# Optimization experiments

Measured on AMD Instinct MI355X. Metric: run time of the kernel, lower is better.

## Reference

```python
import jax, jax.numpy as jnp
import numpy as np

NQ = 12  # qubits == features of M
# (op, theta_offset_or_control, wire_or_target) mirroring TTN_node_forward
CIRCUIT = [
    ("u3", 0, 0), ("u3", 3, 1), ("cx", 0, 1),
    ("u3", 6, 2), ("u3", 9, 3), ("cx", 3, 2),
    ("u3", 12, 4), ("u3", 15, 5), ("cx", 4, 5),
    ("u3", 18, 6), ("u3", 21, 7), ("cx", 7, 6),
    ("u3", 24, 8), ("u3", 27, 9), ("cx", 8, 9),
    ("u3", 30, 10), ("u3", 33, 11), ("cx", 11, 10),
    ("u3", 36, 1), ("u3", 39, 2), ("cx", 1, 2),
    ("u3", 42, 5), ("u3", 45, 6), ("cx", 6, 5),
    ("u3", 48, 9), ("u3", 51, 10), ("cx", 10, 9),
    ("u3", 54, 2), ("u3", 57, 5), ("cx", 2, 5),
    ("u3", 60, 5), ("u3", 63, 9), ("cx", 5, 9),
    ("u3", 66, 4),
]

def _u3(theta, phi, lam):
    ct, st = jnp.cos(theta / 2), jnp.sin(theta / 2)
    r0 = jnp.stack([ct + 0j, -jnp.exp(1j * lam) * st])
    r1 = jnp.stack([jnp.exp(1j * phi) * st, jnp.exp(1j * (phi + lam)) * ct])
    return jnp.stack([r0, r1])  # [2,2] complex64

def _apply_1q(state, U, w):
    # state: (N, 2, ..., 2) with 12 qubit axes; contract U into axis w+1
    out = jnp.tensordot(U, state, axes=((1,), (w + 1,)))
    return jnp.moveaxis(out, 0, w + 1)

def _apply_cnot(state, c, t):
    c_ax, t_ax = c + 1, t + 1
    s0 = jnp.take(state, 0, axis=c_ax)
    s1 = jnp.take(state, 1, axis=c_ax)
    t_adj = t_ax - 1 if t_ax > c_ax else t_ax
    s1 = jnp.flip(s1, axis=t_adj)  # X on target (size-2 axis flip)
    return jnp.stack([s0, s1], axis=c_ax)

def _simulate(M, theta):
    # M: (N, 12) angles; product state from RY(M[:, q]) |0>
    N = M.shape[0]
    state = jnp.ones((N,), dtype=jnp.complex64)
    for q in range(NQ):
        qv = jnp.stack([jnp.cos(M[:, q] / 2), jnp.sin(M[:, q] / 2)], axis=-1)
        qv = qv.astype(jnp.complex64).reshape((N,) + (1,) * q + (2,))
        state = state[..., None] * qv  # (N, 2^(q+1) as axes)
    for op, a, b in CIRCUIT:
        if op == "u3":
            state = _apply_1q(state, _u3(theta[a], theta[a + 1], theta[a + 2]), b)
        else:
            state = _apply_cnot(state, a, b)
    p = jnp.real(state) ** 2 + jnp.imag(state) ** 2  # probabilities
    sum_axes = tuple(ax for ax in range(1, NQ + 1) if ax != 10)  # keep wire 9
    pz = p.sum(axis=sum_axes)  # (N, 2)
    return pz[:, 0] - pz[:, 1]  # <Z_9>

def setup_inputs() -> dict:
    key = jax.random.key(0)
    k1, k2, k3, k4, k5 = jax.random.split(key, 5)
    N, E = 2048, 4096
    X = jax.random.normal(k1, (N, 4), dtype=jnp.float32)
    e = jax.random.uniform(k2, (E,), dtype=jnp.float32)
    Ri = jax.random.uniform(k3, (N, E), dtype=jnp.float32)
    Ro = jax.random.uniform(k4, (N, E), dtype=jnp.float32)
    theta_learn = jax.random.uniform(k5, (69,), dtype=jnp.float32,
                                     minval=0.0, maxval=2.0 * np.pi)
    return {"X": X, "e": e, "Ri": Ri, "Ro": Ro, "theta_learn": theta_learn}

def reference(X, e, Ri, Ro, theta_learn):
    bo = jnp.einsum('ne,nd->ed', Ro, X)          # Ro^T X
    bi = jnp.einsum('ne,nd->ed', Ri, X)          # Ri^T X
    mi = jnp.einsum('ne,ed->nd', Ri * e[None, :], bo)
    mo = jnp.einsum('ne,ed->nd', Ro * e[None, :], bi)
    M = jnp.concatenate([mi, mo, X], axis=1)     # (N, 12)
    z = _simulate(M, theta_learn)
    return jnp.pi * (1.0 - z)                    # 2*pi*(1 - <Z>)/2
```

## Files before the change

kernel.cpp:

```cpp
#include <hip/hip_runtime.h>
#include <math.h>

#define N_SAMPLES 2048
#define E_EDGES   4096
#define NSPLIT    32

__global__ __launch_bounds__(256) void k_partial(const float* __restrict__ Ri,
                                                 const float* __restrict__ Ro,
                                                 const float* __restrict__ X,
                                                 float* __restrict__ pbo,
                                                 float* __restrict__ pbi) {
    __shared__ float comb[128][33];

    const int ec   = blockIdx.x;
    const int ns   = blockIdx.y;
    const int t    = threadIdx.x;
    const int col  = t & 127;
    const int half = t >> 7;
    const int v    = ec * 128 + col;

    const float4* Ri4 = reinterpret_cast<const float4*>(Ri);
    const float4* Ro4 = reinterpret_cast<const float4*>(Ro);
    const float4* X4  = reinterpret_cast<const float4*>(X);

    float abo[4][4], abi[4][4];
#pragma unroll
    for (int c = 0; c < 4; ++c)
#pragma unroll
        for (int d = 0; d < 4; ++d) { abo[c][d] = 0.f; abi[c][d] = 0.f; }

    const int n0 = ns * 64 + half * 32;
    for (int n = n0; n < n0 + 32; ++n) {
        float4 xv = X4[n];
        float4 ro = Ro4[(size_t)n * 1024 + v];
        float4 ri = Ri4[(size_t)n * 1024 + v];
        float xs[4]  = {xv.x, xv.y, xv.z, xv.w};
        float ros[4] = {ro.x, ro.y, ro.z, ro.w};
        float ris[4] = {ri.x, ri.y, ri.z, ri.w};
#pragma unroll
        for (int c = 0; c < 4; ++c)
#pragma unroll
            for (int d = 0; d < 4; ++d) {
                abo[c][d] += ros[c] * xs[d];
                abi[c][d] += ris[c] * xs[d];
            }
    }

    if (half) {
#pragma unroll
        for (int c = 0; c < 4; ++c)
#pragma unroll
            for (int d = 0; d < 4; ++d) {
                comb[col][c * 4 + d]      = abo[c][d];
                comb[col][16 + c * 4 + d] = abi[c][d];
            }
    }
    __syncthreads();
    if (!half) {
        float4* pbo4 = reinterpret_cast<float4*>(pbo);
        float4* pbi4 = reinterpret_cast<float4*>(pbi);
#pragma unroll
        for (int c = 0; c < 4; ++c) {
#pragma unroll
            for (int d = 0; d < 4; ++d) {
                abo[c][d] += comb[col][c * 4 + d];
                abi[c][d] += comb[col][16 + c * 4 + d];
            }
            size_t idx = (size_t)ns * E_EDGES + 4 * (size_t)v + c;
            pbo4[idx] = make_float4(abo[c][0], abo[c][1], abo[c][2], abo[c][3]);
            pbi4[idx] = make_float4(abi[c][0], abi[c][1], abi[c][2], abi[c][3]);
        }
    }
}

__global__ __launch_bounds__(256) void k_reduce(const float* __restrict__ pbo,
                                                const float* __restrict__ pbi,
                                                const float* __restrict__ ev,
                                                float* __restrict__ boT,
                                                float* __restrict__ biT) {
    const int gid = blockIdx.x * 256 + threadIdx.x;
    const int mat = gid >> 12;
    const int e   = gid & 4095;
    const float4* src = reinterpret_cast<const float4*>(mat ? pbi : pbo);
    float*        dst = mat ? biT : boT;
    double s0 = 0, s1 = 0, s2 = 0, s3 = 0;
    for (int ns = 0; ns < NSPLIT; ++ns) {
        float4 a = src[(size_t)ns * E_EDGES + e];
        s0 += a.x; s1 += a.y; s2 += a.z; s3 += a.w;
    }
    const float w = ev[e];
    dst[0 * E_EDGES + e] = w * (float)s0;
    dst[1 * E_EDGES + e] = w * (float)s1;
    dst[2 * E_EDGES + e] = w * (float)s2;
    dst[3 * E_EDGES + e] = w * (float)s3;
}

__global__ __launch_bounds__(256) void k_sim(const float* __restrict__ Ri,
                                             const float* __restrict__ Ro,
                                             const float* __restrict__ X,
                                             const float* __restrict__ th,
                                             const float* __restrict__ boT,
                                             const float* __restrict__ biT,
                                             float* __restrict__ out) {
    __shared__ double redM[4][8];
    __shared__ float  R[22][9];
    __shared__ float  sM[12], cM[12];

    const int n    = blockIdx.x;
    const int t    = threadIdx.x;
    const int lane = t & 63;
    const int wv   = t >> 6;

    if (t < 22) {
        float T = th[3 * t], P = th[3 * t + 1], L = th[3 * t + 2];
        float st, ct, sp, cp, sl, cl;
        sincosf(T, &st, &ct);
        sincosf(P, &sp, &cp);
        sincosf(L, &sl, &cl);
        R[t][0] =  cp * ct * cl - sp * sl;
        R[t][1] = -cp * ct * sl - sp * cl;
        R[t][2] =  cp * st;
        R[t][3] =  sp * ct * cl + cp * sl;
        R[t][4] = -sp * ct * sl + cp * cl;
        R[t][5] =  sp * st;
        R[t][6] = -st * cl;
        R[t][7] =  st * sl;
        R[t][8] =  ct;
    }

    float accf[8];
#pragma unroll
    for (int j = 0; j < 8; ++j) accf[j] = 0.f;

    const float4* Ri4 = reinterpret_cast<const float4*>(Ri + (size_t)n * E_EDGES);
    const float4* Ro4 = reinterpret_cast<const float4*>(Ro + (size_t)n * E_EDGES);
    const float4* BO0 = reinterpret_cast<const float4*>(boT);
    const float4* BO1 = reinterpret_cast<const float4*>(boT + E_EDGES);
    const float4* BO2 = reinterpret_cast<const float4*>(boT + 2 * E_EDGES);
    const float4* BO3 = reinterpret_cast<const float4*>(boT + 3 * E_EDGES);
    const float4* BI0 = reinterpret_cast<const float4*>(biT);
    const float4* BI1 = reinterpret_cast<const float4*>(biT + E_EDGES);
    const float4* BI2 = reinterpret_cast<const float4*>(biT + 2 * E_EDGES);
    const float4* BI3 = reinterpret_cast<const float4*>(biT + 3 * E_EDGES);
#pragma unroll
    for (int k = 0; k < 4; ++k) {
        const int v = t + 256 * k;
        const float4 ri = Ri4[v], ro = Ro4[v];
        const float4 o0 = BO0[v], o1 = BO1[v], o2 = BO2[v], o3 = BO3[v];
        const float4 i0 = BI0[v], i1 = BI1[v], i2 = BI2[v], i3 = BI3[v];
        accf[0] += ri.x * o0.x + ri.y * o0.y + ri.z * o0.z + ri.w * o0.w;
        accf[1] += ri.x * o1.x + ri.y * o1.y + ri.z * o1.z + ri.w * o1.w;
        accf[2] += ri.x * o2.x + ri.y * o2.y + ri.z * o2.z + ri.w * o2.w;
        accf[3] += ri.x * o3.x + ri.y * o3.y + ri.z * o3.z + ri.w * o3.w;
        accf[4] += ro.x * i0.x + ro.y * i0.y + ro.z * i0.z + ro.w * i0.w;
        accf[5] += ro.x * i1.x + ro.y * i1.y + ro.z * i1.z + ro.w * i1.w;
        accf[6] += ro.x * i2.x + ro.y * i2.y + ro.z * i2.z + ro.w * i2.w;
        accf[7] += ro.x * i3.x + ro.y * i3.y + ro.z * i3.z + ro.w * i3.w;
    }
    double accd[8];
#pragma unroll
    for (int j = 0; j < 8; ++j) accd[j] = (double)accf[j];
#pragma unroll
    for (int off = 32; off >= 1; off >>= 1)
#pragma unroll
        for (int j = 0; j < 8; ++j) accd[j] += __shfl_xor(accd[j], off);
    if (lane == 0)
#pragma unroll
        for (int j = 0; j < 8; ++j) redM[wv][j] = accd[j];
    __syncthreads();

    if (t < 12) {
        double Mw = (t < 8)
            ? (redM[0][t] + redM[1][t] + redM[2][t] + redM[3][t])
            : (double)X[n * 4 + (t - 8)];
        double sv, cv;
        sincos(Mw, &sv, &cv);
        sM[t] = (float)sv; cM[t] = (float)cv;
    }
    __syncthreads();

    if (t == 0) {
        auto iz = [&](int g) -> float {
            return R[g][6] * sM[g] + R[g][8] * cM[g];
        };
        auto ivec = [&](int g, float& x, float& y, float& z) {
            x = R[g][0] * sM[g] + R[g][2] * cM[g];
            y = R[g][3] * sM[g] + R[g][5] * cM[g];
            z = R[g][6] * sM[g] + R[g][8] * cM[g];
        };
        auto rot = [&](int g, float& x, float& y, float& z) {
            float nx = R[g][0] * x + R[g][1] * y + R[g][2] * z;
            float ny = R[g][3] * x + R[g][4] * y + R[g][5] * z;
            float nz = R[g][6] * x + R[g][7] * y + R[g][8] * z;
            x = nx; y = ny; z = nz;
        };

        const float z0  = iz(0),  z3  = iz(3), z4 = iz(4);
        const float z7  = iz(7),  z8  = iz(8), z11 = iz(11);

        float x1, y1, z1;  ivec(1, x1, y1, z1);
        y1 *= z0;  z1 *= z0;          rot(12, x1, y1, z1);

        float x2, y2, z2;  ivec(2, x2, y2, z2);
        y2 *= z3;  z2 *= z3;          rot(13, x2, y2, z2);
        y2 *= z1;  z2 *= z1;          rot(18, x2, y2, z2);

        float x6, y6, z6;  ivec(6, x6, y6, z6);
        y6 *= z7;  z6 *= z7;          rot(15, x6, y6, z6);

        float x5, y5, z5;  ivec(5, x5, y5, z5);
        y5 *= z4;  z5 *= z4;          rot(14, x5, y5, z5);
        y5 *= z6;  z5 *= z6;          rot(19, x5, y5, z5);
        y5 *= z2;  z5 *= z2;          rot(20, x5, y5, z5);

        float xA, yA, zA;  ivec(10, xA, yA, zA);
        yA *= z11; zA *= z11;         rot(17, xA, yA, zA);

        float x9, y9, z9;  ivec(9, x9, y9, z9);
        y9 *= z8;  z9 *= z8;          rot(16, x9, y9, z9);
        y9 *= zA;  z9 *= zA;          rot(21, x9, y9, z9);
        z9 *= z5;

        out[n] = (float)(3.14159265358979323846 * (1.0 - (double)z9));
    }
}

extern "C" void kernel_launch(void* const* d_in, const int* in_sizes, int n_in,
                              void* d_out, int out_size, void* d_ws, size_t ws_size,
                              hipStream_t stream) {
    (void)in_sizes; (void)n_in; (void)out_size; (void)ws_size;
    const float* X  = (const float*)d_in[0];
    const float* ev = (const float*)d_in[1];
    const float* Ri = (const float*)d_in[2];
    const float* Ro = (const float*)d_in[3];
    const float* th = (const float*)d_in[4];
    float* out = (float*)d_out;

    float* pbo = (float*)d_ws;
    float* pbi = pbo + (size_t)NSPLIT * E_EDGES * 4;
    float* boT = pbi + (size_t)NSPLIT * E_EDGES * 4;
    float* biT = boT + (size_t)4 * E_EDGES;

    hipLaunchKernelGGL(k_partial, dim3(8, NSPLIT), dim3(256), 0, stream,
                       Ri, Ro, X, pbo, pbi);
    hipLaunchKernelGGL(k_reduce, dim3(32), dim3(256), 0, stream,
                       pbo, pbi, ev, boT, biT);
    hipLaunchKernelGGL(k_sim, dim3(N_SAMPLES), dim3(256), 0, stream,
                       Ri, Ro, X, th, boT, biT, out);
}
```

Before: 41.13 us.

## Split partial sums finer, parallelize reduce across lanes, batch samples per sim block

Doubles the N-split of the partial Ro^T X / Ri^T X kernel to 64 chunks so more blocks run in parallel. The reduce kernel gets four lanes per edge, each summing 16 partials in float, combined with shuffles; the float accumulation replaces double. The sim kernel now handles four samples per block, loading boT/biT once and reusing them across samples, which cuts redundant reads of the shared vectors. The workspace for partials grows, and the lower-precision reduction may slightly change numerics.

New measurement: 43.13 us. 4.9% more time.

```diff
diff --git a/kernel.cpp b/kernel.cpp
--- a/kernel.cpp
+++ b/kernel.cpp
@@ -3,7 +3,8 @@
 
 #define N_SAMPLES 2048
 #define E_EDGES   4096
-#define NSPLIT    32
+#define NSPLIT    64
+#define SPB       4
 
 __global__ __launch_bounds__(256) void k_partial(const float* __restrict__ Ri,
                                                  const float* __restrict__ Ro,
@@ -29,8 +30,9 @@
 #pragma unroll
         for (int d = 0; d < 4; ++d) { abo[c][d] = 0.f; abi[c][d] = 0.f; }
 
-    const int n0 = ns * 64 + half * 32;
-    for (int n = n0; n < n0 + 32; ++n) {
+    const int n0 = ns * 32 + half * 16;
+#pragma unroll 4
+    for (int n = n0; n < n0 + 16; ++n) {
         float4 xv = X4[n];
         float4 ro = Ro4[(size_t)n * 1024 + v];
         float4 ri = Ri4[(size_t)n * 1024 + v];
@@ -79,20 +81,29 @@
                                                 float* __restrict__ boT,
                                                 float* __restrict__ biT) {
     const int gid = blockIdx.x * 256 + threadIdx.x;
-    const int mat = gid >> 12;
-    const int e   = gid & 4095;
+    const int q   = gid & 3;
+    const int e   = (gid >> 2) & 4095;
+    const int mat = gid >> 14;
     const float4* src = reinterpret_cast<const float4*>(mat ? pbi : pbo);
     float*        dst = mat ? biT : boT;
-    double s0 = 0, s1 = 0, s2 = 0, s3 = 0;
-    for (int ns = 0; ns < NSPLIT; ++ns) {
+
+    float s0 = 0.f, s1 = 0.f, s2 = 0.f, s3 = 0.f;
+#pragma unroll 4
+    for (int ns = q * 16; ns < q * 16 + 16; ++ns) {
         float4 a = src[(size_t)ns * E_EDGES + e];
         s0 += a.x; s1 += a.y; s2 += a.z; s3 += a.w;
     }
-    const float w = ev[e];
-    dst[0 * E_EDGES + e] = w * (float)s0;
-    dst[1 * E_EDGES + e] = w * (float)s1;
-    dst[2 * E_EDGES + e] = w * (float)s2;
-    dst[3 * E_EDGES + e] = w * (float)s3;
+    s0 += __shfl_xor(s0, 1); s0 += __shfl_xor(s0, 2);
+    s1 += __shfl_xor(s1, 1); s1 += __shfl_xor(s1, 2);
+    s2 += __shfl_xor(s2, 1); s2 += __shfl_xor(s2, 2);
+    s3 += __shfl_xor(s3, 1); s3 += __shfl_xor(s3, 2);
+    if (q == 0) {
+        const float w = ev[e];
+        dst[0 * E_EDGES + e] = w * s0;
+        dst[1 * E_EDGES + e] = w * s1;
+        dst[2 * E_EDGES + e] = w * s2;
+        dst[3 * E_EDGES + e] = w * s3;
+    }
 }
 
 __global__ __launch_bounds__(256) void k_sim(const float* __restrict__ Ri,
@@ -102,11 +113,11 @@
                                              const float* __restrict__ boT,
                                              const float* __restrict__ biT,
                                              float* __restrict__ out) {
-    __shared__ double redM[4][8];
+    __shared__ double redM[4][SPB][8];
     __shared__ float  R[22][9];
-    __shared__ float  sM[12], cM[12];
-
-    const int n    = blockIdx.x;
+    __shared__ float  sM[SPB][12], cM[SPB][12];
+
+    const int n0   = blockIdx.x * SPB;
     const int t    = threadIdx.x;
     const int lane = t & 63;
     const int wv   = t >> 6;
@@ -128,12 +139,19 @@
         R[t][8] =  ct;
     }
 
-    float accf[8];
-#pragma unroll
-    for (int j = 0; j < 8; ++j) accf[j] = 0.f;
-
-    const float4* Ri4 = reinterpret_cast<const float4*>(Ri + (size_t)n * E_EDGES);
-    const float4* Ro4 = reinterpret_cast<const float4*>(Ro + (size_t)n * E_EDGES);
+    float accf[SPB][8];
+#pragma unroll
+    for (int s = 0; s < SPB; ++s)
+#pragma unroll
+        for (int j = 0; j < 8; ++j) accf[s][j] = 0.f;
+
+    const float4* Ri4s[SPB];
+    const float4* Ro4s[SPB];
+#pragma unroll
+    for (int s = 0; s < SPB; ++s) {
+        Ri4s[s] = reinterpret_cast<const float4*>(Ri + (size_t)(n0 + s) * E_EDGES);
+        Ro4s[s] = reinterpret_cast<const float4*>(Ro + (size_t)(n0 + s) * E_EDGES);
+    }
     const float4* BO0 = reinterpret_cast<const float4*>(boT);
     const float4* BO1 = reinterpret_cast<const float4*>(boT + E_EDGES);
     const float4* BO2 = reinterpret_cast<const float4*>(boT + 2 * E_EDGES);
@@ -142,51 +160,67 @@
     const float4* BI1 = reinterpret_cast<const float4*>(biT + E_EDGES);
     const float4* BI2 = reinterpret_cast<const float4*>(biT + 2 * E_EDGES);
     const float4* BI3 = reinterpret_cast<const float4*>(biT + 3 * E_EDGES);
+
 #pragma unroll
     for (int k = 0; k < 4; ++k) {
         const int v = t + 256 * k;
-        const float4 ri = Ri4[v], ro = Ro4[v];
         const float4 o0 = BO0[v], o1 = BO1[v], o2 = BO2[v], o3 = BO3[v];
         const float4 i0 = BI0[v], i1 = BI1[v], i2 = BI2[v], i3 = BI3[v];
-        accf[0] += ri.x * o0.x + ri.y * o0.y + ri.z * o0.z + ri.w * o0.w;
-        accf[1] += ri.x * o1.x + ri.y * o1.y + ri.z * o1.z + ri.w * o1.w;
-        accf[2] += ri.x * o2.x + ri.y * o2.y + ri.z * o2.z + ri.w * o2.w;
-        accf[3] += ri.x * o3.x + ri.y * o3.y + ri.z * o3.z + ri.w * o3.w;
-        accf[4] += ro.x * i0.x + ro.y * i0.y + ro.z * i0.z + ro.w * i0.w;
-        accf[5] += ro.x * i1.x + ro.y * i1.y + ro.z * i1.z + ro.w * i1.w;
-        accf[6] += ro.x * i2.x + ro.y * i2.y + ro.z * i2.z + ro.w * i2.w;
-        accf[7] += ro.x * i3.x + ro.y * i3.y + ro.z * i3.z + ro.w * i3.w;
-    }
-    double accd[8];
-#pragma unroll
-    for (int j = 0; j < 8; ++j) accd[j] = (double)accf[j];
+#pragma unroll
+        for (int s = 0; s < SPB; ++s) {
+            const float4 ri = Ri4s[s][v];
+            const float4 ro = Ro4s[s][v];
+            accf[s][0] += ri.x * o0.x + ri.y * o0.y + ri.z * o0.z + ri.w * o0.w;
+            accf[s][1] += ri.x * o1.x + ri.y * o1.y + ri.z * o1.z + ri.w * o1.w;
+            accf[s][2] += ri.x * o2.x + ri.y * o2.y + ri.z * o2.z + ri.w * o2.w;
+            accf[s][3] += ri.x * o3.x + ri.y * o3.y + ri.z * o3.z + ri.w * o3.w;
+            accf[s][4] += ro.x * i0.x + ro.y * i0.y + ro.z * i0.z + ro.w * i0.w;
+            accf[s][5] += ro.x * i1.x + ro.y * i1.y + ro.z * i1.z + ro.w * i1.w;
+            accf[s][6] += ro.x * i2.x + ro.y * i2.y + ro.z * i2.z + ro.w * i2.w;
+            accf[s][7] += ro.x * i3.x + ro.y * i3.y + ro.z * i3.z + ro.w * i3.w;
+        }
+    }
+
+    double accd[SPB][8];
+#pragma unroll
+    for (int s = 0; s < SPB; ++s)
+#pragma unroll
+        for (int j = 0; j < 8; ++j) accd[s][j] = (double)accf[s][j];
 #pragma unroll
     for (int off = 32; off >= 1; off >>= 1)
 #pragma unroll
-        for (int j = 0; j < 8; ++j) accd[j] += __shfl_xor(accd[j], off);
+        for (int s = 0; s < SPB; ++s)
+#pragma unroll
+            for (int j = 0; j < 8; ++j)
+                accd[s][j] += __shfl_xor(accd[s][j], off);
     if (lane == 0)
 #pragma unroll
-        for (int j = 0; j < 8; ++j) redM[wv][j] = accd[j];
+        for (int s = 0; s < SPB; ++s)
+#pragma unroll
+            for (int j = 0; j < 8; ++j) redM[wv][s][j] = accd[s][j];
     __syncthreads();
 
-    if (t < 12) {
-        double Mw = (t < 8)
-            ? (redM[0][t] + redM[1][t] + redM[2][t] + redM[3][t])
-            : (double)X[n * 4 + (t - 8)];
+    if (t < 12 * SPB) {
+        const int s = t / 12, w = t % 12;
+        double Mw = (w < 8)
+            ? (redM[0][s][w] + redM[1][s][w] + redM[2][s][w] + redM[3][s][w])
+            : (double)X[(n0 + s) * 4 + (w - 8)];
         double sv, cv;
         sincos(Mw, &sv, &cv);
-        sM[t] = (float)sv; cM[t] = (float)cv;
+        sM[s][w] = (float)sv; cM[s][w] = (float)cv;
     }
     __syncthreads();
 
-    if (t == 0) {
+    if (t < SPB) {
+        const float* sMv = sM[t];
+        const float* cMv = cM[t];
         auto iz = [&](int g) -> float {
-            return R[g][6] * sM[g] + R[g][8] * cM[g];
+            return R[g][6] * sMv[g] + R[g][8] * cMv[g];
         };
         auto ivec = [&](int g, float& x, float& y, float& z) {
-            x = R[g][0] * sM[g] + R[g][2] * cM[g];
-            y = R[g][3] * sM[g] + R[g][5] * cM[g];
-            z = R[g][6] * sM[g] + R[g][8] * cM[g];
+            x = R[g][0] * sMv[g] + R[g][2] * cMv[g];
+            y = R[g][3] * sMv[g] + R[g][5] * cMv[g];
+            z = R[g][6] * sMv[g] + R[g][8] * cMv[g];
         };
         auto rot = [&](int g, float& x, float& y, float& z) {
             float nx = R[g][0] * x + R[g][1] * y + R[g][2] * z;
@@ -221,7 +255,7 @@
         y9 *= zA;  z9 *= zA;          rot(21, x9, y9, z9);
         z9 *= z5;
 
-        out[n] = (float)(3.14159265358979323846 * (1.0 - (double)z9));
+        out[n0 + t] = (float)(3.14159265358979323846 * (1.0 - (double)z9));
     }
 }
 
@@ -243,8 +277,8 @@
 
     hipLaunchKernelGGL(k_partial, dim3(8, NSPLIT), dim3(256), 0, stream,
                        Ri, Ro, X, pbo, pbi);
-    hipLaunchKernelGGL(k_reduce, dim3(32), dim3(256), 0, stream,
+    hipLaunchKernelGGL(k_reduce, dim3(128), dim3(256), 0, stream,
                        pbo, pbi, ev, boT, biT);
-    hipLaunchKernelGGL(k_sim, dim3(N_SAMPLES), dim3(256), 0, stream,
+    hipLaunchKernelGGL(k_sim, dim3(N_SAMPLES / SPB), dim3(256), 0, stream,
                        Ri, Ro, X, th, boT, biT, out);
 }
```
